# Performance work log

Hardware: AMD Instinct MI355X
Metric: run time of the kernel (lower is better)

## Reference

```python
import jax, jax.numpy as jnp
import numpy as np

DT = 0.5  # timestep; CFL-stable for c<1, grid spacing h=1


def laplace5(u):
    # 5-point Laplacian with zero (Dirichlet) boundary, grid spacing 1.
    # u: [B, Nx, Ny]
    z = jnp.pad(u, ((0, 0), (1, 1), (1, 1)))
    return (z[:, 2:, 1:-1] + z[:, :-2, 1:-1]
            + z[:, 1:-1, 2:] + z[:, 1:-1, :-2] - 4.0 * u)


def setup_inputs() -> dict:
    key = jax.random.key(0)
    k1, k2, k3, k4, k5 = jax.random.split(key, 5)
    B, T, Nx, Ny, Np = 16, 256, 256, 256, 3
    x = jax.random.normal(k1, (B, T), dtype=jnp.float32)
    c = jax.random.uniform(k2, (Nx, Ny), dtype=jnp.float32)      # wave speed
    b = jax.random.uniform(k3, (Nx, Ny), dtype=jnp.float32)      # damping (rho)
    px = jax.random.randint(k4, (Np,), 0, Nx)
    py = jax.random.randint(k5, (Np,), 0, Ny)
    return {"x": x, "c": c, "b": b, "px": px, "py": py, "sx": 128, "sy": 128}


def reference(x, c, b, px, py, sx, sy):
    # x: [B, T], c,b: [Nx, Ny]; returns y: [B, T, Np]
    B = x.shape[0]
    Nx, Ny = c.shape
    c1 = 1.0 / (1.0 + 0.5 * DT * b)          # [Nx, Ny]
    c2 = 1.0 - 0.5 * DT * b                  # [Nx, Ny]
    csq_dt2 = (DT * DT) * (c * c)            # [Nx, Ny]
    h0 = jnp.zeros((B, Nx, Ny), dtype=x.dtype)

    def step(carry, xi):
        h1, h2 = carry
        # wave cell: second-order leapfrog with damping
        hn = c1 * (2.0 * h1 - c2 * h2 + csq_dt2 * laplace5(h1))
        # point source injection of scalar input per batch element
        hn = hn.at[:, sx, sy].add(xi)
        # point probes -> [B, Np]
        y = hn[:, px, py]
        return (hn, h1), y

    xt = jnp.transpose(x, (1, 0))            # [T, B]
    _, ys = jax.lax.scan(step, (h0, h0), xt)  # ys: [T, B, Np]
    return jnp.transpose(ys, (1, 0, 2))       # [B, T, Np]
```

## Files before the change

kernel.cpp:

```cpp
#include <hip/hip_runtime.h>


#define B_    16
#define T_    256
#define NY    256
#define NP    3
#define NSLAB 8
#define WAVES 8
#define THREADS 512
#define NIF   (NSLAB - 1)

__device__ uint64_t g_halo[2][B_][NIF][2][4][64];

__global__ void reset_halo()
{
    const int n = 2 * B_ * NIF * 2 * 4 * 64;
    int i = blockIdx.x * blockDim.x + threadIdx.x;
    if (i < n) (&g_halo[0][0][0][0][0][0])[i] = 0ull;
}

#define PACK(tag, f) (((uint64_t)(uint32_t)(tag) << 32) | (uint64_t)__float_as_uint(f))

#define GPOLL(dst, side, iface, P_, TT) do { \
    uint64_t* gp_ = &g_halo[side][b][iface][P_][0][l]; \
    uint64_t a0_, a1_, a2_, a3_; bool ok_; \
    do { \
        a0_ = __hip_atomic_load(gp_ + 0 * 64, __ATOMIC_RELAXED, __HIP_MEMORY_SCOPE_AGENT); \
        a1_ = __hip_atomic_load(gp_ + 1 * 64, __ATOMIC_RELAXED, __HIP_MEMORY_SCOPE_AGENT); \
        a2_ = __hip_atomic_load(gp_ + 2 * 64, __ATOMIC_RELAXED, __HIP_MEMORY_SCOPE_AGENT); \
        a3_ = __hip_atomic_load(gp_ + 3 * 64, __ATOMIC_RELAXED, __HIP_MEMORY_SCOPE_AGENT); \
        ok_ = ((uint32_t)(a0_ >> 32) == (uint32_t)(TT)) && ((uint32_t)(a1_ >> 32) == (uint32_t)(TT)) \
           && ((uint32_t)(a2_ >> 32) == (uint32_t)(TT)) && ((uint32_t)(a3_ >> 32) == (uint32_t)(TT)); \
    } while (!ok_); \
    dst[0] = __uint_as_float((uint32_t)a0_); dst[1] = __uint_as_float((uint32_t)a1_); \
    dst[2] = __uint_as_float((uint32_t)a2_); dst[3] = __uint_as_float((uint32_t)a3_); \
} while (0)

#define GPUB(side, iface, Q_, TAG1, HROW) do { \
    uint64_t* gp_ = &g_halo[side][b][iface][Q_][0][l]; \
    __hip_atomic_store(gp_ + 0 * 64, PACK(TAG1, HROW[0]), __ATOMIC_RELAXED, __HIP_MEMORY_SCOPE_AGENT); \
    __hip_atomic_store(gp_ + 1 * 64, PACK(TAG1, HROW[1]), __ATOMIC_RELAXED, __HIP_MEMORY_SCOPE_AGENT); \
    __hip_atomic_store(gp_ + 2 * 64, PACK(TAG1, HROW[2]), __ATOMIC_RELAXED, __HIP_MEMORY_SCOPE_AGENT); \
    __hip_atomic_store(gp_ + 3 * 64, PACK(TAG1, HROW[3]), __ATOMIC_RELAXED, __HIP_MEMORY_SCOPE_AGENT); \
} while (0)

#define ROWC(H1, H2, r, UPA, DNA) do { \
    float lf_ = __shfl_up(H1[r][3], 1, 64); \
    float rt_ = __shfl_down(H1[r][0], 1, 64); \
    if (l == 0)  lf_ = 0.f; \
    if (l == 63) rt_ = 0.f; \
    _Pragma("unroll") for (int j = 0; j < 4; ++j) { \
        const float lv_ = (j == 0) ? lf_ : H1[r][j - 1]; \
        const float rv_ = (j == 3) ? rt_ : H1[r][j + 1]; \
        const float s4_ = (UPA[j] + DNA[j]) + (lv_ + rv_); \
        const float d_  = H1[r][j] - H2[r][j]; \
        const float e_  = fmaf(-4.0f, H1[r][j], s4_); \
        float v_ = fmaf(CC[r][j], e_, H2[r][j]); \
        v_ = fmaf(TC[r][j], d_, v_); \
        H2[r][j] = v_; \
    } \
} while (0)

#define SRCP(H2, r, TT) do { \
    if (srcHere && src_r == (r)) { \
        _Pragma("unroll") for (int j = 0; j < 4; ++j) \
            if (src_c == j) H2[r][j] += xbuf[TT]; \
    } \
    _Pragma("unroll") for (int qq = 0; qq < NP; ++qq) { \
        if (pHere[qq] && pr[qq] == (r)) { \
            float v_ = 0.f; \
            _Pragma("unroll") for (int j = 0; j < 4; ++j) \
                if (pc[qq] == j) v_ = H2[r][j]; \
            out[((size_t)b * T_ + (TT)) * NP + qq] = v_; \
        } \
    } \
} while (0)

#define SUB(H1, H2, TT, P_, Q_) do { \
    float gu_[4], gd_[4]; \
    if (w == 0) { \
        if (s == 0) { gu_[0] = gu_[1] = gu_[2] = gu_[3] = 0.f; } \
        else GPOLL(gu_, 0, s - 1, P_, TT); \
    } else { \
        while (__hip_atomic_load(&r3t[w - 1][P_], __ATOMIC_RELAXED, __HIP_MEMORY_SCOPE_WORKGROUP) != (TT)) {} \
        asm volatile("" ::: "memory"); \
        const float4 u4_ = *reinterpret_cast<const float4*>(&r3v[w - 1][P_][y0]); \
        gu_[0] = u4_.x; gu_[1] = u4_.y; gu_[2] = u4_.z; gu_[3] = u4_.w; \
    } \
    if (w == WAVES - 1) { \
        if (s == NSLAB - 1) { gd_[0] = gd_[1] = gd_[2] = gd_[3] = 0.f; } \
        else GPOLL(gd_, 1, s, P_, TT); \
    } else { \
        while (__hip_atomic_load(&r0t[w + 1][P_], __ATOMIC_RELAXED, __HIP_MEMORY_SCOPE_WORKGROUP) != (TT)) {} \
        asm volatile("" ::: "memory"); \
        const float4 d4_ = *reinterpret_cast<const float4*>(&r0v[w + 1][P_][y0]); \
        gd_[0] = d4_.x; gd_[1] = d4_.y; gd_[2] = d4_.z; gd_[3] = d4_.w; \
    } \
     \
    ROWC(H1, H2, 0, gu_, H1[1]); \
    ROWC(H1, H2, 3, H1[2], gd_); \
    SRCP(H2, 0, TT); \
    SRCP(H2, 3, TT); \
     \
    if (w > 0) \
        *reinterpret_cast<float4*>(&r0v[w][Q_][y0]) = make_float4(H2[0][0], H2[0][1], H2[0][2], H2[0][3]); \
    if (w < WAVES - 1) \
        *reinterpret_cast<float4*>(&r3v[w][Q_][y0]) = make_float4(H2[3][0], H2[3][1], H2[3][2], H2[3][3]); \
    asm volatile("s_waitcnt lgkmcnt(0)" ::: "memory"); \
    if (l == 0) { \
        if (w > 0) \
            __hip_atomic_store(&r0t[w][Q_], (TT) + 1, __ATOMIC_RELAXED, __HIP_MEMORY_SCOPE_WORKGROUP); \
        if (w < WAVES - 1) \
            __hip_atomic_store(&r3t[w][Q_], (TT) + 1, __ATOMIC_RELAXED, __HIP_MEMORY_SCOPE_WORKGROUP); \
    } \
    if (w == 0 && s > 0)                 GPUB(1, s - 1, Q_, (TT) + 1, H2[0]); \
    if (w == WAVES - 1 && s < NSLAB - 1) GPUB(0, s,     Q_, (TT) + 1, H2[3]); \
     \
    ROWC(H1, H2, 1, H1[0], H1[2]); \
    ROWC(H1, H2, 2, H1[1], H1[3]); \
    SRCP(H2, 1, TT); \
    SRCP(H2, 2, TT); \
} while (0)

__launch_bounds__(THREADS, 2)
__global__ void wave_multi(const float* __restrict__ xin,
                           const float* __restrict__ cin,
                           const float* __restrict__ bin,
                           const int* __restrict__ pxp,
                           const int* __restrict__ pyp,
                           const int* __restrict__ sxp,
                           const int* __restrict__ syp,
                           float* __restrict__ out)
{
    const int blk = blockIdx.x;
    const int b = blk >> 3;
    const int s = blk & 7;
    const int tid = threadIdx.x;
    const int w = tid >> 6;
    const int l = tid & 63;
    const int r0 = s * 32 + w * 4;
    const int y0 = l * 4;

    __shared__ float xbuf[T_];
    __shared__ float r0v[WAVES][2][NY];
    __shared__ float r3v[WAVES][2][NY];
    __shared__ int   r0t[WAVES][2];
    __shared__ int   r3t[WAVES][2];

    for (int i = tid; i < WAVES * 2 * NY; i += THREADS) {
        (&r0v[0][0][0])[i] = 0.f;
        (&r3v[0][0][0])[i] = 0.f;
    }
    if (tid < WAVES * 2) {
        const int w_ = tid >> 1, p_ = tid & 1;
        r0t[w_][p_] = (p_ == 0) ? 0 : -1;
        r3t[w_][p_] = (p_ == 0) ? 0 : -1;
    }
    if (tid < T_) xbuf[tid] = xin[b * T_ + tid];

    float h1[4][4], h2[4][4], TC[4][4], CC[4][4];
#pragma unroll
    for (int r = 0; r < 4; ++r) {
        const float4 cv = *reinterpret_cast<const float4*>(&cin[(r0 + r) * NY + y0]);
        const float4 bv = *reinterpret_cast<const float4*>(&bin[(r0 + r) * NY + y0]);
        const float cvv[4] = {cv.x, cv.y, cv.z, cv.w};
        const float bvv[4] = {bv.x, bv.y, bv.z, bv.w};
#pragma unroll
        for (int j = 0; j < 4; ++j) {
            const float c1  = 1.0f / (1.0f + 0.25f * bvv[j]);
            const float csq = 0.25f * cvv[j] * cvv[j];
            TC[r][j] = 2.0f * c1;
            CC[r][j] = c1 * csq;
            h1[r][j] = 0.f;
            h2[r][j] = 0.f;
        }
    }

    const int sx = sxp[0], sy = syp[0];
    const bool srcHere = (sx >= r0 && sx < r0 + 4 && sy >= y0 && sy < y0 + 4);
    const int  src_r = sx - r0, src_c = sy - y0;
    bool pHere[NP];
    int  pr[NP], pc[NP];
#pragma unroll
    for (int q = 0; q < NP; ++q) {
        const int pxx = pxp[q], pyy = pyp[q];
        pHere[q] = (pxx >= r0 && pxx < r0 + 4 && pyy >= y0 && pyy < y0 + 4);
        pr[q] = pxx - r0;
        pc[q] = pyy - y0;
    }

    __syncthreads();

#pragma unroll 1
    for (int t = 0; t < T_; t += 2) {
        SUB(h1, h2, t,     0, 1);
        SUB(h2, h1, t + 1, 1, 0);
    }
}

extern "C" void kernel_launch(void* const* d_in, const int* in_sizes, int n_in,
                              void* d_out, int out_size, void* d_ws, size_t ws_size,
                              hipStream_t stream)
{
    const float* x  = (const float*)d_in[0];
    const float* c  = (const float*)d_in[1];
    const float* bb = (const float*)d_in[2];
    const int*   px = (const int*)d_in[3];
    const int*   py = (const int*)d_in[4];
    const int*   sx = (const int*)d_in[5];
    const int*   sy = (const int*)d_in[6];
    float* out = (float*)d_out;

    const int words = 2 * B_ * NIF * 2 * 4 * 64;
    reset_halo<<<(words + 255) / 256, 256, 0, stream>>>();

    void* args[] = { (void*)&x, (void*)&c, (void*)&bb, (void*)&px, (void*)&py,
                     (void*)&sx, (void*)&sy, (void*)&out };
    hipLaunchCooperativeKernel(reinterpret_cast<void*>(wave_multi),
                               dim3(B_ * NSLAB), dim3(THREADS), args, 0, stream);
}
```

Baseline: 358.7 us.

## Use temporal blocking with 4-step halo exchange chunks and redundant ghost-row compute

Replaces per-timestep halo exchange between waves and slabs with chunks of four timesteps. Each wave holds four ghost rows on each side and recomputes them redundantly, shrinking the valid region each step. Halo data is exchanged through LDS with two block barriers per chunk, and across blocks through tagged global atomics, 32 values per lane. The goal is fewer synchronisation round trips, paid for with extra redundant stencil work, more registers (launch bounds drop to one block per CU) and larger global polls.

```diff
diff --git a/kernel.cpp b/kernel.cpp
--- a/kernel.cpp
+++ b/kernel.cpp
@@ -9,120 +9,146 @@
 #define WAVES 8
 #define THREADS 512
 #define NIF   (NSLAB - 1)
-
-__device__ uint64_t g_halo[2][B_][NIF][2][4][64];
+#define KCH   4
+#define NCHUNK (T_ / KCH)
+
+__device__ uint64_t g_halo[B_][NIF][2][2][8][NY];
 
 __global__ void reset_halo()
 {
-    const int n = 2 * B_ * NIF * 2 * 4 * 64;
+    const int n = B_ * NIF * 2 * 2 * 8 * NY;
     int i = blockIdx.x * blockDim.x + threadIdx.x;
     if (i < n) (&g_halo[0][0][0][0][0][0])[i] = 0ull;
 }
 
 #define PACK(tag, f) (((uint64_t)(uint32_t)(tag) << 32) | (uint64_t)__float_as_uint(f))
 
-#define GPOLL(dst, side, iface, P_, TT) do { \
-    uint64_t* gp_ = &g_halo[side][b][iface][P_][0][l]; \
-    uint64_t a0_, a1_, a2_, a3_; bool ok_; \
+#define GPOLL32(GA, GB, SIDE, IFACE, TAG) do { \
+    uint64_t* gp_ = &g_halo[b][IFACE][SIDE][(TAG) & 1][0][0]; \
+    uint64_t vv_[8][4]; bool ok_; \
     do { \
-        a0_ = __hip_atomic_load(gp_ + 0 * 64, __ATOMIC_RELAXED, __HIP_MEMORY_SCOPE_AGENT); \
-        a1_ = __hip_atomic_load(gp_ + 1 * 64, __ATOMIC_RELAXED, __HIP_MEMORY_SCOPE_AGENT); \
-        a2_ = __hip_atomic_load(gp_ + 2 * 64, __ATOMIC_RELAXED, __HIP_MEMORY_SCOPE_AGENT); \
-        a3_ = __hip_atomic_load(gp_ + 3 * 64, __ATOMIC_RELAXED, __HIP_MEMORY_SCOPE_AGENT); \
-        ok_ = ((uint32_t)(a0_ >> 32) == (uint32_t)(TT)) && ((uint32_t)(a1_ >> 32) == (uint32_t)(TT)) \
-           && ((uint32_t)(a2_ >> 32) == (uint32_t)(TT)) && ((uint32_t)(a3_ >> 32) == (uint32_t)(TT)); \
+        ok_ = true; \
+        _Pragma("unroll") for (int rf = 0; rf < 8; ++rf) \
+            _Pragma("unroll") for (int j = 0; j < 4; ++j) \
+                vv_[rf][j] = __hip_atomic_load(gp_ + rf * NY + j * 64 + l, \
+                                               __ATOMIC_RELAXED, __HIP_MEMORY_SCOPE_AGENT); \
+        _Pragma("unroll") for (int rf = 0; rf < 8; ++rf) \
+            _Pragma("unroll") for (int j = 0; j < 4; ++j) \
+                ok_ = ok_ && ((uint32_t)(vv_[rf][j] >> 32) == (uint32_t)(TAG)); \
     } while (!ok_); \
-    dst[0] = __uint_as_float((uint32_t)a0_); dst[1] = __uint_as_float((uint32_t)a1_); \
-    dst[2] = __uint_as_float((uint32_t)a2_); dst[3] = __uint_as_float((uint32_t)a3_); \
-} while (0)
-
-#define GPUB(side, iface, Q_, TAG1, HROW) do { \
-    uint64_t* gp_ = &g_halo[side][b][iface][Q_][0][l]; \
-    __hip_atomic_store(gp_ + 0 * 64, PACK(TAG1, HROW[0]), __ATOMIC_RELAXED, __HIP_MEMORY_SCOPE_AGENT); \
-    __hip_atomic_store(gp_ + 1 * 64, PACK(TAG1, HROW[1]), __ATOMIC_RELAXED, __HIP_MEMORY_SCOPE_AGENT); \
-    __hip_atomic_store(gp_ + 2 * 64, PACK(TAG1, HROW[2]), __ATOMIC_RELAXED, __HIP_MEMORY_SCOPE_AGENT); \
-    __hip_atomic_store(gp_ + 3 * 64, PACK(TAG1, HROW[3]), __ATOMIC_RELAXED, __HIP_MEMORY_SCOPE_AGENT); \
-} while (0)
-
-#define ROWC(H1, H2, r, UPA, DNA) do { \
-    float lf_ = __shfl_up(H1[r][3], 1, 64); \
-    float rt_ = __shfl_down(H1[r][0], 1, 64); \
+    _Pragma("unroll") for (int i = 0; i < 4; ++i) \
+        _Pragma("unroll") for (int j = 0; j < 4; ++j) { \
+            GA[i][j] = __uint_as_float((uint32_t)vv_[i][j]); \
+            GB[i][j] = __uint_as_float((uint32_t)vv_[4 + i][j]); \
+        } \
+} while (0)
+
+#define GPUB32(SIDE, IFACE, TAG1, HH1, HH2) do { \
+    uint64_t* gp_ = &g_halo[b][IFACE][SIDE][(TAG1) & 1][0][0]; \
+    _Pragma("unroll") for (int i = 0; i < 4; ++i) \
+        _Pragma("unroll") for (int j = 0; j < 4; ++j) { \
+            __hip_atomic_store(gp_ + i * NY + j * 64 + l, PACK(TAG1, HH1[i][j]), \
+                               __ATOMIC_RELAXED, __HIP_MEMORY_SCOPE_AGENT); \
+            __hip_atomic_store(gp_ + (4 + i) * NY + j * 64 + l, PACK(TAG1, HH2[i][j]), \
+                               __ATOMIC_RELAXED, __HIP_MEMORY_SCOPE_AGENT); \
+        } \
+} while (0)
+
+#define ROWC(HA, HB, r, UPA, DNA) do { \
+    float lf_ = __shfl_up(HA[r][3], 1, 64); \
+    float rt_ = __shfl_down(HA[r][0], 1, 64); \
     if (l == 0)  lf_ = 0.f; \
     if (l == 63) rt_ = 0.f; \
     _Pragma("unroll") for (int j = 0; j < 4; ++j) { \
-        const float lv_ = (j == 0) ? lf_ : H1[r][j - 1]; \
-        const float rv_ = (j == 3) ? rt_ : H1[r][j + 1]; \
+        const float lv_ = (j == 0) ? lf_ : HA[r][j - 1]; \
+        const float rv_ = (j == 3) ? rt_ : HA[r][j + 1]; \
         const float s4_ = (UPA[j] + DNA[j]) + (lv_ + rv_); \
-        const float d_  = H1[r][j] - H2[r][j]; \
-        const float e_  = fmaf(-4.0f, H1[r][j], s4_); \
-        float v_ = fmaf(CC[r][j], e_, H2[r][j]); \
-        v_ = fmaf(TC[r][j], d_, v_); \
-        H2[r][j] = v_; \
-    } \
-} while (0)
-
-#define SRCP(H2, r, TT) do { \
+        const float d_  = HA[r][j] - HB[r][j]; \
+        const float e_  = fmaf(-4.0f, HA[r][j], s4_); \
+        float v_ = fmaf(CCr[r][j], e_, HB[r][j]); \
+        v_ = fmaf(TCr[r][j], d_, v_); \
+        HB[r][j] = v_; \
+    } \
+} while (0)
+
+#define SRCP(HB, r, TT) do { \
     if (srcHere && src_r == (r)) { \
         _Pragma("unroll") for (int j = 0; j < 4; ++j) \
-            if (src_c == j) H2[r][j] += xbuf[TT]; \
+            if (src_c == j) HB[r][j] += xbuf[TT]; \
     } \
     _Pragma("unroll") for (int qq = 0; qq < NP; ++qq) { \
         if (pHere[qq] && pr[qq] == (r)) { \
             float v_ = 0.f; \
             _Pragma("unroll") for (int j = 0; j < 4; ++j) \
-                if (pc[qq] == j) v_ = H2[r][j]; \
+                if (pc[qq] == j) v_ = HB[r][j]; \
             out[((size_t)b * T_ + (TT)) * NP + qq] = v_; \
         } \
     } \
 } while (0)
 
-#define SUB(H1, H2, TT, P_, Q_) do { \
-    float gu_[4], gd_[4]; \
-    if (w == 0) { \
-        if (s == 0) { gu_[0] = gu_[1] = gu_[2] = gu_[3] = 0.f; } \
-        else GPOLL(gu_, 0, s - 1, P_, TT); \
-    } else { \
-        while (__hip_atomic_load(&r3t[w - 1][P_], __ATOMIC_RELAXED, __HIP_MEMORY_SCOPE_WORKGROUP) != (TT)) {} \
-        asm volatile("" ::: "memory"); \
-        const float4 u4_ = *reinterpret_cast<const float4*>(&r3v[w - 1][P_][y0]); \
-        gu_[0] = u4_.x; gu_[1] = u4_.y; gu_[2] = u4_.z; gu_[3] = u4_.w; \
-    } \
-    if (w == WAVES - 1) { \
-        if (s == NSLAB - 1) { gd_[0] = gd_[1] = gd_[2] = gd_[3] = 0.f; } \
-        else GPOLL(gd_, 1, s, P_, TT); \
-    } else { \
-        while (__hip_atomic_load(&r0t[w + 1][P_], __ATOMIC_RELAXED, __HIP_MEMORY_SCOPE_WORKGROUP) != (TT)) {} \
-        asm volatile("" ::: "memory"); \
-        const float4 d4_ = *reinterpret_cast<const float4*>(&r0v[w + 1][P_][y0]); \
-        gd_[0] = d4_.x; gd_[1] = d4_.y; gd_[2] = d4_.z; gd_[3] = d4_.w; \
-    } \
-     \
-    ROWC(H1, H2, 0, gu_, H1[1]); \
-    ROWC(H1, H2, 3, H1[2], gd_); \
-    SRCP(H2, 0, TT); \
-    SRCP(H2, 3, TT); \
-     \
-    if (w > 0) \
-        *reinterpret_cast<float4*>(&r0v[w][Q_][y0]) = make_float4(H2[0][0], H2[0][1], H2[0][2], H2[0][3]); \
-    if (w < WAVES - 1) \
-        *reinterpret_cast<float4*>(&r3v[w][Q_][y0]) = make_float4(H2[3][0], H2[3][1], H2[3][2], H2[3][3]); \
-    asm volatile("s_waitcnt lgkmcnt(0)" ::: "memory"); \
-    if (l == 0) { \
-        if (w > 0) \
-            __hip_atomic_store(&r0t[w][Q_], (TT) + 1, __ATOMIC_RELAXED, __HIP_MEMORY_SCOPE_WORKGROUP); \
-        if (w < WAVES - 1) \
-            __hip_atomic_store(&r3t[w][Q_], (TT) + 1, __ATOMIC_RELAXED, __HIP_MEMORY_SCOPE_WORKGROUP); \
-    } \
-    if (w == 0 && s > 0)                 GPUB(1, s - 1, Q_, (TT) + 1, H2[0]); \
-    if (w == WAVES - 1 && s < NSLAB - 1) GPUB(0, s,     Q_, (TT) + 1, H2[3]); \
-     \
-    ROWC(H1, H2, 1, H1[0], H1[2]); \
-    ROWC(H1, H2, 2, H1[1], H1[3]); \
-    SRCP(H2, 1, TT); \
-    SRCP(H2, 2, TT); \
-} while (0)
-
-__launch_bounds__(THREADS, 2)
+#define GUP(GA, GB, HA, I_, K_, TT) do { \
+    if ((I_) >= (K_) + 1) { \
+        const float4 tc4_ = *reinterpret_cast<const float4*>(&ldsTC[w4 + (I_)][y0]); \
+        const float4 cc4_ = *reinterpret_cast<const float4*>(&ldsCC[w4 + (I_)][y0]); \
+        const float tcv_[4] = {tc4_.x, tc4_.y, tc4_.z, tc4_.w}; \
+        const float ccv_[4] = {cc4_.x, cc4_.y, cc4_.z, cc4_.w}; \
+        float lf_ = __shfl_up(GA[I_][3], 1, 64); \
+        float rt_ = __shfl_down(GA[I_][0], 1, 64); \
+        if (l == 0)  lf_ = 0.f; \
+        if (l == 63) rt_ = 0.f; \
+        _Pragma("unroll") for (int j = 0; j < 4; ++j) { \
+            const float lv_ = (j == 0) ? lf_ : GA[I_][j - 1]; \
+            const float rv_ = (j == 3) ? rt_ : GA[I_][j + 1]; \
+            const float av_ = GA[I_ - 1][j]; \
+            const float dv_ = ((I_) == 3) ? HA[0][j] : GA[I_ + 1][j]; \
+            const float s4_ = (av_ + dv_) + (lv_ + rv_); \
+            const float d_  = GA[I_][j] - GB[I_][j]; \
+            const float e_  = fmaf(-4.0f, GA[I_][j], s4_); \
+            float v_ = fmaf(ccv_[j], e_, GB[I_][j]); \
+            v_ = fmaf(tcv_[j], d_, v_); \
+            if (srcUp && gsu_r == (I_) && gsu_c == j) v_ += xbuf[TT]; \
+            GB[I_][j] = v_; \
+        } \
+    } \
+} while (0)
+
+#define GDN(GA, GB, HA, I_, K_, TT) do { \
+    if ((I_) <= 2 - (K_)) { \
+        const float4 tc4_ = *reinterpret_cast<const float4*>(&ldsTC[w4 + 8 + (I_)][y0]); \
+        const float4 cc4_ = *reinterpret_cast<const float4*>(&ldsCC[w4 + 8 + (I_)][y0]); \
+        const float tcv_[4] = {tc4_.x, tc4_.y, tc4_.z, tc4_.w}; \
+        const float ccv_[4] = {cc4_.x, cc4_.y, cc4_.z, cc4_.w}; \
+        float lf_ = __shfl_up(GA[I_][3], 1, 64); \
+        float rt_ = __shfl_down(GA[I_][0], 1, 64); \
+        if (l == 0)  lf_ = 0.f; \
+        if (l == 63) rt_ = 0.f; \
+        _Pragma("unroll") for (int j = 0; j < 4; ++j) { \
+            const float lv_ = (j == 0) ? lf_ : GA[I_][j - 1]; \
+            const float rv_ = (j == 3) ? rt_ : GA[I_][j + 1]; \
+            const float av_ = ((I_) == 0) ? HA[3][j] : GA[I_ - 1][j]; \
+            const float dv_ = GA[I_ + 1][j]; \
+            const float s4_ = (av_ + dv_) + (lv_ + rv_); \
+            const float d_  = GA[I_][j] - GB[I_][j]; \
+            const float e_  = fmaf(-4.0f, GA[I_][j], s4_); \
+            float v_ = fmaf(ccv_[j], e_, GB[I_][j]); \
+            v_ = fmaf(tcv_[j], d_, v_); \
+            if (srcDn && gsd_r == (I_) && gsd_c == j) v_ += xbuf[TT]; \
+            GB[I_][j] = v_; \
+        } \
+    } \
+} while (0)
+
+#define SUBK(HA, HB, GUA, GUB, GDA, GDB, K_, TT) do { \
+    ROWC(HA, HB, 0, GUA[3], HA[1]); \
+    ROWC(HA, HB, 1, HA[0],  HA[2]); \
+    ROWC(HA, HB, 2, HA[1],  HA[3]); \
+    ROWC(HA, HB, 3, HA[2],  GDA[0]); \
+    SRCP(HB, 0, TT); SRCP(HB, 1, TT); SRCP(HB, 2, TT); SRCP(HB, 3, TT); \
+    if (hasUp) { GUP(GUA, GUB, HA, 1, K_, TT); GUP(GUA, GUB, HA, 2, K_, TT); GUP(GUA, GUB, HA, 3, K_, TT); } \
+    if (hasDn) { GDN(GDA, GDB, HA, 0, K_, TT); GDN(GDA, GDB, HA, 1, K_, TT); GDN(GDA, GDB, HA, 2, K_, TT); } \
+} while (0)
+
+__launch_bounds__(THREADS, 1)
 __global__ void wave_multi(const float* __restrict__ xin,
                            const float* __restrict__ cin,
                            const float* __restrict__ bin,
@@ -138,47 +164,61 @@
     const int tid = threadIdx.x;
     const int w = tid >> 6;
     const int l = tid & 63;
+    const int w4 = w << 2;
     const int r0 = s * 32 + w * 4;
     const int y0 = l * 4;
 
+    __shared__ float ldsTC[40][NY];
+    __shared__ float ldsCC[40][NY];
+    __shared__ float ldsHalo[WAVES][8][NY];
     __shared__ float xbuf[T_];
-    __shared__ float r0v[WAVES][2][NY];
-    __shared__ float r3v[WAVES][2][NY];
-    __shared__ int   r0t[WAVES][2];
-    __shared__ int   r3t[WAVES][2];
-
-    for (int i = tid; i < WAVES * 2 * NY; i += THREADS) {
-        (&r0v[0][0][0])[i] = 0.f;
-        (&r3v[0][0][0])[i] = 0.f;
-    }
-    if (tid < WAVES * 2) {
-        const int w_ = tid >> 1, p_ = tid & 1;
-        r0t[w_][p_] = (p_ == 0) ? 0 : -1;
-        r3t[w_][p_] = (p_ == 0) ? 0 : -1;
-    }
+
+    for (int e = tid; e < 40 * NY; e += THREADS) {
+        const int row = e >> 8, col = e & 255;
+        int grow = s * 32 - 4 + row;
+        grow = grow < 0 ? 0 : (grow > 255 ? 255 : grow);
+        const float cv = cin[grow * NY + col];
+        const float bv = bin[grow * NY + col];
+        const float c1  = 1.0f / (1.0f + 0.25f * bv);
+        const float csq = 0.25f * cv * cv;
+        ldsTC[row][col] = 2.0f * c1;
+        ldsCC[row][col] = c1 * csq;
+    }
+    for (int e = tid; e < WAVES * 8 * NY; e += THREADS)
+        (&ldsHalo[0][0][0])[e] = 0.f;
     if (tid < T_) xbuf[tid] = xin[b * T_ + tid];
-
-    float h1[4][4], h2[4][4], TC[4][4], CC[4][4];
+    __syncthreads();
+
+    float TCr[4][4], CCr[4][4], h1[4][4], h2[4][4];
 #pragma unroll
     for (int r = 0; r < 4; ++r) {
-        const float4 cv = *reinterpret_cast<const float4*>(&cin[(r0 + r) * NY + y0]);
-        const float4 bv = *reinterpret_cast<const float4*>(&bin[(r0 + r) * NY + y0]);
-        const float cvv[4] = {cv.x, cv.y, cv.z, cv.w};
-        const float bvv[4] = {bv.x, bv.y, bv.z, bv.w};
+        const float4 t4 = *reinterpret_cast<const float4*>(&ldsTC[w4 + 4 + r][y0]);
+        const float4 c4 = *reinterpret_cast<const float4*>(&ldsCC[w4 + 4 + r][y0]);
+        TCr[r][0] = t4.x; TCr[r][1] = t4.y; TCr[r][2] = t4.z; TCr[r][3] = t4.w;
+        CCr[r][0] = c4.x; CCr[r][1] = c4.y; CCr[r][2] = c4.z; CCr[r][3] = c4.w;
+#pragma unroll
+        for (int j = 0; j < 4; ++j) { h1[r][j] = 0.f; h2[r][j] = 0.f; }
+    }
+
+    float gu_a[4][4], gu_b[4][4], gd_a[4][4], gd_b[4][4];
+#pragma unroll
+    for (int i = 0; i < 4; ++i)
 #pragma unroll
         for (int j = 0; j < 4; ++j) {
-            const float c1  = 1.0f / (1.0f + 0.25f * bvv[j]);
-            const float csq = 0.25f * cvv[j] * cvv[j];
-            TC[r][j] = 2.0f * c1;
-            CC[r][j] = c1 * csq;
-            h1[r][j] = 0.f;
-            h2[r][j] = 0.f;
-        }
-    }
+            gu_a[i][j] = 0.f; gu_b[i][j] = 0.f;
+            gd_a[i][j] = 0.f; gd_b[i][j] = 0.f;
+        }
+
+    const bool hasUp = (w > 0) || (s > 0);
+    const bool hasDn = (w < WAVES - 1) || (s < NSLAB - 1);
 
     const int sx = sxp[0], sy = syp[0];
     const bool srcHere = (sx >= r0 && sx < r0 + 4 && sy >= y0 && sy < y0 + 4);
     const int  src_r = sx - r0, src_c = sy - y0;
+    const bool srcUp = hasUp && (sx >= r0 - 4 && sx < r0     && sy >= y0 && sy < y0 + 4);
+    const int  gsu_r = sx - (r0 - 4), gsu_c = sy - y0;
+    const bool srcDn = hasDn && (sx >= r0 + 4 && sx < r0 + 8 && sy >= y0 && sy < y0 + 4);
+    const int  gsd_r = sx - (r0 + 4), gsd_c = sy - y0;
     bool pHere[NP];
     int  pr[NP], pc[NP];
 #pragma unroll
@@ -189,12 +229,50 @@
         pc[q] = pyy - y0;
     }
 
-    __syncthreads();
-
 #pragma unroll 1
-    for (int t = 0; t < T_; t += 2) {
-        SUB(h1, h2, t,     0, 1);
-        SUB(h2, h1, t + 1, 1, 0);
+    for (int c = 0; c < NCHUNK; ++c) {
+        if (w > 0) {
+#pragma unroll
+            for (int i = 0; i < 4; ++i) {
+                const float4 a4 = *reinterpret_cast<const float4*>(&ldsHalo[w - 1][i][y0]);
+                const float4 b4 = *reinterpret_cast<const float4*>(&ldsHalo[w - 1][4 + i][y0]);
+                gu_a[i][0] = a4.x; gu_a[i][1] = a4.y; gu_a[i][2] = a4.z; gu_a[i][3] = a4.w;
+                gu_b[i][0] = b4.x; gu_b[i][1] = b4.y; gu_b[i][2] = b4.z; gu_b[i][3] = b4.w;
+            }
+        } else if (s > 0) {
+            GPOLL32(gu_a, gu_b, 0, s - 1, c);
+        }
+        if (w < WAVES - 1) {
+#pragma unroll
+            for (int i = 0; i < 4; ++i) {
+                const float4 a4 = *reinterpret_cast<const float4*>(&ldsHalo[w + 1][i][y0]);
+                const float4 b4 = *reinterpret_cast<const float4*>(&ldsHalo[w + 1][4 + i][y0]);
+                gd_a[i][0] = a4.x; gd_a[i][1] = a4.y; gd_a[i][2] = a4.z; gd_a[i][3] = a4.w;
+                gd_b[i][0] = b4.x; gd_b[i][1] = b4.y; gd_b[i][2] = b4.z; gd_b[i][3] = b4.w;
+            }
+        } else if (s < NSLAB - 1) {
+            GPOLL32(gd_a, gd_b, 1, s, c);
+        }
+        __syncthreads();
+
+        const int t4 = 4 * c;
+        SUBK(h1, h2, gu_a, gu_b, gd_a, gd_b, 0, t4 + 0);
+        SUBK(h2, h1, gu_b, gu_a, gd_b, gd_a, 1, t4 + 1);
+        SUBK(h1, h2, gu_a, gu_b, gd_a, gd_b, 2, t4 + 2);
+        SUBK(h2, h1, gu_b, gu_a, gd_b, gd_a, 3, t4 + 3);
+
+#pragma unroll
+        for (int i = 0; i < 4; ++i) {
+            *reinterpret_cast<float4*>(&ldsHalo[w][i][y0]) =
+                make_float4(h1[i][0], h1[i][1], h1[i][2], h1[i][3]);
+            *reinterpret_cast<float4*>(&ldsHalo[w][4 + i][y0]) =
+                make_float4(h2[i][0], h2[i][1], h2[i][2], h2[i][3]);
+        }
+        if (c + 1 < NCHUNK) {
+            if (w == 0 && s > 0)                 GPUB32(1, s - 1, c + 1, h1, h2);
+            if (w == WAVES - 1 && s < NSLAB - 1) GPUB32(0, s,     c + 1, h1, h2);
+        }
+        __syncthreads();
     }
 }
 
@@ -211,7 +289,7 @@
     const int*   sy = (const int*)d_in[6];
     float* out = (float*)d_out;
 
-    const int words = 2 * B_ * NIF * 2 * 4 * 64;
+    const int words = B_ * NIF * 2 * 2 * 8 * NY;
     reset_halo<<<(words + 255) / 256, 256, 0, stream>>>();
 
     void* args[] = { (void*)&x, (void*)&c, (void*)&bb, (void*)&px, (void*)&py,
```

New measurement: 493.4 us. 1.38x slower.
